# Kernel tuning notes

Measured on AMD Instinct MI355X. Metric: run time of the kernel, lower is better.

## Reference

```python
import jax, jax.numpy as jnp
import numpy as np
from jax import lax

B = 8192      # image batch
S = 32        # seq_length
I = 16        # ltc_input_size (sensory neurons)
U = 19        # ltc_hidden_size (units)
M = 2         # num_classes (motor neurons)
UNFOLDS = 6   # ncps LTCCell default ode_unfolds
EPS = 1e-8


def setup_inputs() -> dict:
    key = jax.random.key(0)
    ks = jax.random.split(key, 24)
    u = lambda k, sh, lo, hi: jax.random.uniform(k, sh, jnp.float32, lo, hi)
    x = jax.random.normal(ks[0], (B, 1, 28, 44), jnp.float32)
    conv1_w = jax.random.normal(ks[1], (6, 1, 5, 5), jnp.float32) * 0.2
    conv1_b = u(ks[2], (6,), -0.1, 0.1)
    conv2_w = jax.random.normal(ks[3], (16, 6, 5, 5), jnp.float32) * 0.08
    conv2_b = u(ks[4], (16,), -0.1, 0.1)
    # wiring adjacency (AutoNCP approximated by random sparse +/-1 polarity)
    sparsity_mask = (jax.random.uniform(ks[5], (U, U)) < 0.5).astype(jnp.float32)
    sensory_sparsity_mask = (jax.random.uniform(ks[6], (I, U)) < 0.5).astype(jnp.float32)
    erev = sparsity_mask * jnp.where(jax.random.uniform(ks[7], (U, U)) < 0.8, 1.0, -1.0)
    sensory_erev = sensory_sparsity_mask * jnp.where(jax.random.uniform(ks[8], (I, U)) < 0.8, 1.0, -1.0)
    # LTCCell parameter init ranges from ncps
    gleak = u(ks[9], (U,), 0.001, 1.0)
    vleak = u(ks[10], (U,), -0.2, 0.2)
    cm = u(ks[11], (U,), 0.4, 0.6)
    sigma = u(ks[12], (U, U), 3.0, 8.0)
    mu = u(ks[13], (U, U), 0.3, 0.8)
    w = u(ks[14], (U, U), 0.001, 1.0)
    sensory_sigma = u(ks[15], (I, U), 3.0, 8.0)
    sensory_mu = u(ks[16], (I, U), 0.3, 0.8)
    sensory_w = u(ks[17], (I, U), 0.001, 1.0)
    input_w = jnp.ones((I,), jnp.float32)
    input_b = jnp.zeros((I,), jnp.float32)
    output_w = jnp.ones((M,), jnp.float32)
    output_b = jnp.zeros((M,), jnp.float32)
    return dict(x=x, conv1_w=conv1_w, conv1_b=conv1_b, conv2_w=conv2_w, conv2_b=conv2_b,
                gleak=gleak, vleak=vleak, cm=cm, sigma=sigma, mu=mu, w=w, erev=erev,
                sensory_sigma=sensory_sigma, sensory_mu=sensory_mu, sensory_w=sensory_w,
                sensory_erev=sensory_erev, input_w=input_w, input_b=input_b,
                output_w=output_w, output_b=output_b,
                sparsity_mask=sparsity_mask, sensory_sparsity_mask=sensory_sparsity_mask)


def _maxpool2(h):
    return lax.reduce_window(h, -jnp.inf, lax.max, (1, 1, 2, 2), (1, 1, 2, 2), 'VALID')


def reference(x, conv1_w, conv1_b, conv2_w, conv2_b, gleak, vleak, cm, sigma, mu, w,
              erev, sensory_sigma, sensory_mu, sensory_w, sensory_erev, input_w, input_b,
              output_w, output_b, sparsity_mask, sensory_sparsity_mask):
    dn = ('NCHW', 'OIHW', 'NCHW')
    h = lax.conv_general_dilated(x, conv1_w, (1, 1), 'VALID', dimension_numbers=dn)
    h = _maxpool2(jax.nn.relu(h + conv1_b[None, :, None, None]))
    h = lax.conv_general_dilated(h, conv2_w, (1, 1), 'VALID', dimension_numbers=dn)
    h = _maxpool2(jax.nn.relu(h + conv2_b[None, :, None, None]))
    feat = h.reshape(h.shape[0], -1).reshape(-1, S, I)   # (B, 32, 16)
    seq = jnp.swapaxes(feat, 0, 1)                       # (S, B, I)
    cm_t = cm * UNFOLDS                                  # cm / (elapsed_time/unfolds), dt=1

    def step(v, inp):
        inp = inp * input_w + input_b                    # sensory affine mapping
        # sensory synapse activations (B, I, U), fixed over the ODE unfolds
        s_act = sensory_w * jax.nn.sigmoid(sensory_sigma * (inp[:, :, None] - sensory_mu))
        s_act = s_act * sensory_sparsity_mask
        w_num_s = jnp.sum(s_act * sensory_erev, axis=1)
        w_den_s = jnp.sum(s_act, axis=1)

        def unfold(vv, _):
            wa = w * jax.nn.sigmoid(sigma * (vv[:, :, None] - mu)) * sparsity_mask  # (B,U,U)
            num = cm_t * vv + gleak * vleak + jnp.sum(wa * erev, axis=1) + w_num_s
            den = cm_t + gleak + jnp.sum(wa, axis=1) + w_den_s
            return num / (den + EPS), None

        v, _ = lax.scan(unfold, v, None, length=UNFOLDS)
        return v, None

    v0 = jnp.zeros((feat.shape[0], U), x.dtype)
    vT, _ = lax.scan(step, v0, seq)
    # motor mapping: first M neurons, affine output map; equals out[:, -1, :]
    return vT[:, :M] * output_w + output_b
```

## Files before the change

kernel.cpp:

```cpp
#include <hip/hip_runtime.h>

#define BTOT 8192
#define SEQ 32
#define IPB 6
#define TPB 128
#define L2E 1.4426950408889634f
#define FSTRIDE 520
#define VSTRIDE 20

__global__ void prep_w2t(const float* __restrict__ w2, float* __restrict__ wt) {
    int idx = blockIdx.x * blockDim.x + threadIdx.x;
    if (idx < 2400) {
        int k = idx >> 4, c2 = idx & 15;
        wt[idx] = w2[c2 * 150 + k];
    }
}

__global__ __launch_bounds__(TPB, 3) void ltc_fused(
    const float* __restrict__ xin,
    const float* __restrict__ w1, const float* __restrict__ b1,
    const float* __restrict__ b2,
    const float* __restrict__ gleak, const float* __restrict__ vleak, const float* __restrict__ cm,
    const float* __restrict__ sigma, const float* __restrict__ mu, const float* __restrict__ ww,
    const float* __restrict__ erev,
    const float* __restrict__ ssigma, const float* __restrict__ smu, const float* __restrict__ sw,
    const float* __restrict__ serev,
    const float* __restrict__ inw, const float* __restrict__ inb,
    const float* __restrict__ outw, const float* __restrict__ outb,
    const float* __restrict__ mask, const float* __restrict__ smask,
    const float* __restrict__ wt,
    float* __restrict__ dout)
{
    __shared__ __align__(16) float uni[2736];
    __shared__ __align__(16) float featL[IPB * FSTRIDE];
    __shared__ __align__(16) float vbuf[IPB * VSTRIDE];
    __shared__ int ncol[19], mcol[19], cnts[2];

    float* img = uni;
    float* c1p = uni + 1232;
    float4* cR = (float4*)uni;
    float4* cS = ((float4*)uni) + 20 * 19;

    const int tid = threadIdx.x;
    const int b0 = blockIdx.x * IPB;

    for (int k = 0; k < IPB; ++k) {
        const int bG = b0 + k;
        const bool valid = bG < BTOT;
        if (valid) {
            for (int idx = tid; idx < 1232; idx += TPB) img[idx] = xin[bG * 1232 + idx];
        }
        __syncthreads();
        if (valid) {
            for (int idx = tid; idx < 240; idx += TPB) {
                int y = idx / 20, xx = idx - (idx / 20) * 20;
                const float* ib = img + (2 * y) * 44 + 2 * xx;
                float win[6][6];
                #pragma unroll
                for (int r = 0; r < 6; ++r) {
                    float2 a = *(const float2*)(ib + r * 44);
                    float2 b = *(const float2*)(ib + r * 44 + 2);
                    float2 c = *(const float2*)(ib + r * 44 + 4);
                    win[r][0] = a.x; win[r][1] = a.y; win[r][2] = b.x;
                    win[r][3] = b.y; win[r][4] = c.x; win[r][5] = c.y;
                }
                for (int ch = 0; ch < 6; ++ch) {
                    const float* wp = w1 + ch * 25;
                    float a00 = 0.f, a01 = 0.f, a10 = 0.f, a11 = 0.f;
                    #pragma unroll
                    for (int ky = 0; ky < 5; ++ky)
                        #pragma unroll
                        for (int kx = 0; kx < 5; ++kx) {
                            float wv = wp[ky * 5 + kx];
                            a00 = fmaf(wv, win[ky][kx], a00);
                            a01 = fmaf(wv, win[ky][kx + 1], a01);
                            a10 = fmaf(wv, win[ky + 1][kx], a10);
                            a11 = fmaf(wv, win[ky + 1][kx + 1], a11);
                        }
                    float m = fmaxf(fmaxf(a00, a01), fmaxf(a10, a11)) + b1[ch];
                    c1p[ch * 240 + idx] = fmaxf(m, 0.f);
                }
            }
        }
        __syncthreads();
        if (valid) {
            const int oy = tid >> 4, ox = tid & 15;
            float acc[16];
            #pragma unroll
            for (int c2 = 0; c2 < 16; ++c2) acc[c2] = 0.f;
            for (int ch = 0; ch < 6; ++ch) {
                const float* rowb = c1p + ch * 240 + oy * 20 + ox;
                const float* wch = wt + (ch * 25 << 4);
                #pragma unroll
                for (int ky = 0; ky < 5; ++ky) {
                    #pragma unroll
                    for (int kx = 0; kx < 5; ++kx) {
                        float xv = rowb[ky * 20 + kx];
                        const float4* wk = (const float4*)(wch + ((ky * 5 + kx) << 4));
                        float4 wa = wk[0], wb = wk[1], wc = wk[2], wd = wk[3];
                        acc[0]  = fmaf(wa.x, xv, acc[0]);  acc[1]  = fmaf(wa.y, xv, acc[1]);
                        acc[2]  = fmaf(wa.z, xv, acc[2]);  acc[3]  = fmaf(wa.w, xv, acc[3]);
                        acc[4]  = fmaf(wb.x, xv, acc[4]);  acc[5]  = fmaf(wb.y, xv, acc[5]);
                        acc[6]  = fmaf(wb.z, xv, acc[6]);  acc[7]  = fmaf(wb.w, xv, acc[7]);
                        acc[8]  = fmaf(wc.x, xv, acc[8]);  acc[9]  = fmaf(wc.y, xv, acc[9]);
                        acc[10] = fmaf(wc.z, xv, acc[10]); acc[11] = fmaf(wc.w, xv, acc[11]);
                        acc[12] = fmaf(wd.x, xv, acc[12]); acc[13] = fmaf(wd.y, xv, acc[13]);
                        acc[14] = fmaf(wd.z, xv, acc[14]); acc[15] = fmaf(wd.w, xv, acc[15]);
                    }
                }
            }
            const bool wl = ((tid & 1) == 0) && ((tid & 16) == 0);
            const int obase = k * FSTRIDE + (oy >> 1) * 8 + (ox >> 1);
            #pragma unroll
            for (int c2 = 0; c2 < 16; ++c2) {
                float a = acc[c2];
                a = fmaxf(a, __shfl_xor(a, 1));
                a = fmaxf(a, __shfl_xor(a, 16));
                if (wl) featL[obase + c2 * 32] = fmaxf(a + b2[c2], 0.f);
            }
        }
        __syncthreads();
    }

    for (int idx = tid; idx < 2736; idx += TPB) uni[idx] = 0.f;
    if (tid < IPB * VSTRIDE) vbuf[tid] = 0.f;
    __syncthreads();
    if (tid < 19) {
        const int j = tid;
        int c = 0;
        for (int i = 0; i < 19; ++i) {
            int idx = i * 19 + j;
            if (mask[idx] != 0.f) {
                float s = sigma[idx];
                cR[c * 19 + j] = make_float4(-L2E * s, L2E * s * mu[idx],
                                             ww[idx] * erev[idx], __int_as_float(i * 4));
                ++c;
            }
        }
        ncol[j] = c;
        c = 0;
        for (int i = 0; i < 16; ++i) {
            int idx = i * 19 + j;
            if (smask[idx] != 0.f) {
                float s = ssigma[idx];
                cS[c * 19 + j] = make_float4(-L2E * s * inw[i],
                                             -L2E * s * (inb[i] - smu[idx]),
                                             sw[idx] * serev[idx], __int_as_float(i * 4));
                ++c;
            }
        }
        mcol[j] = c;
    }
    __syncthreads();
    if (tid == 0) {
        int MR = 0, MS = 0;
        for (int j2 = 0; j2 < 19; ++j2) {
            MR = max(MR, ncol[j2]);
            MS = max(MS, mcol[j2]);
        }
        cnts[0] = (MR + 1) & ~1;
        cnts[1] = (MS + 1) & ~1;
    }
    __syncthreads();
    const int MR = __builtin_amdgcn_readfirstlane(cnts[0]);
    const int MS = __builtin_amdgcn_readfirstlane(cnts[1]);

    const int wv_ = tid >> 6, l = tid & 63;
    const int g = l / 19;
    const int j = l - g * 19;
    const int kimg = wv_ * 3 + g;
    const bool act = (g < 3) && (b0 + kimg < BTOT);
    const int kc = (kimg < IPB) ? kimg : (IPB - 1);

    const float gl = gleak[j];
    const float gv = gl * vleak[j];
    const float cmt = cm[j] * 6.f;

    float v = 0.f;
    const char* frowb = (const char*)(featL + kc * FSTRIDE);
    const char* vrowb = (const char*)(vbuf + kc * VSTRIDE);

    #pragma unroll 1
    for (int st = 0; st < SEQ; ++st) {
        const char* fb = frowb + (st << 6);
        float wns = 0.f, wds = 0.f;
        #pragma unroll 1
        for (int c = 0; c < MS; c += 2) {
            float4 pa = cS[c * 19 + j];
            float4 pb = cS[(c + 1) * 19 + j];
            float fa = *(const float*)(fb + __float_as_int(pa.w));
            float fbv = *(const float*)(fb + __float_as_int(pb.w));
            float ta = fmaf(pa.x, fa, pa.y);
            float tb = fmaf(pb.x, fbv, pb.y);
            float qa = 1.f + __builtin_amdgcn_exp2f(ta);
            float qb = 1.f + __builtin_amdgcn_exp2f(tb);
            float rr = __builtin_amdgcn_rcpf(qa * qb);
            float cn = fmaf(pa.z, qb, pb.z * qa);
            float cd = fmaf(fabsf(pa.z), qb, fabsf(pb.z) * qa);
            wns = fmaf(cn, rr, wns);
            wds = fmaf(cd, rr, wds);
        }
        const float nb = gv + wns;
        const float db = cmt + gl + wds;
        #pragma unroll 1
        for (int u = 0; u < 6; ++u) {
            float num = fmaf(cmt, v, nb);
            float den = db;
            #pragma unroll 1
            for (int c = 0; c < MR; c += 2) {
                float4 pa = cR[c * 19 + j];
                float4 pb = cR[(c + 1) * 19 + j];
                float va = *(const float*)(vrowb + __float_as_int(pa.w));
                float vb = *(const float*)(vrowb + __float_as_int(pb.w));
                float ta = fmaf(pa.x, va, pa.y);
                float tb = fmaf(pb.x, vb, pb.y);
                float qa = 1.f + __builtin_amdgcn_exp2f(ta);
                float qb = 1.f + __builtin_amdgcn_exp2f(tb);
                float rr = __builtin_amdgcn_rcpf(qa * qb);
                float cn = fmaf(pa.z, qb, pb.z * qa);
                float cd = fmaf(fabsf(pa.z), qb, fabsf(pb.z) * qa);
                num = fmaf(cn, rr, num);
                den = fmaf(cd, rr, den);
            }
            v = num * __builtin_amdgcn_rcpf(den + 1e-8f);
            __builtin_amdgcn_wave_barrier();
            __asm__ volatile("" ::: "memory");
            if (act) vbuf[kimg * VSTRIDE + j] = v;
            __builtin_amdgcn_wave_barrier();
            __asm__ volatile("" ::: "memory");
        }
    }
    if (act && j < 2) dout[(b0 + kimg) * 2 + j] = fmaf(v, outw[j], outb[j]);
}

extern "C" void kernel_launch(void* const* d_in, const int* in_sizes, int n_in,
                              void* d_out, int out_size, void* d_ws, size_t ws_size,
                              hipStream_t stream) {
    const float* x      = (const float*)d_in[0];
    const float* w1     = (const float*)d_in[1];
    const float* b1     = (const float*)d_in[2];
    const float* w2     = (const float*)d_in[3];
    const float* b2     = (const float*)d_in[4];
    const float* gleak  = (const float*)d_in[5];
    const float* vleak  = (const float*)d_in[6];
    const float* cm     = (const float*)d_in[7];
    const float* sigma  = (const float*)d_in[8];
    const float* mu     = (const float*)d_in[9];
    const float* ww     = (const float*)d_in[10];
    const float* erev   = (const float*)d_in[11];
    const float* ssig   = (const float*)d_in[12];
    const float* smu    = (const float*)d_in[13];
    const float* sw     = (const float*)d_in[14];
    const float* serev  = (const float*)d_in[15];
    const float* inw    = (const float*)d_in[16];
    const float* inb    = (const float*)d_in[17];
    const float* outw   = (const float*)d_in[18];
    const float* outb   = (const float*)d_in[19];
    const float* mask   = (const float*)d_in[20];
    const float* smask  = (const float*)d_in[21];
    float* wt = (float*)d_ws;

    hipLaunchKernelGGL(prep_w2t, dim3(10), dim3(256), 0, stream, w2, wt);

    dim3 grid((BTOT + IPB - 1) / IPB), block(TPB);
    hipLaunchKernelGGL(ltc_fused, grid, block, 0, stream,
                       x, w1, b1, b2, gleak, vleak, cm, sigma, mu, ww, erev,
                       ssig, smu, sw, serev, inw, inb, outw, outb, mask, smask,
                       (const float*)wt, (float*)d_out);
}
```

Measured before the change: 359.6 us.

## Cache recurrent synapse params in registers and exchange state via shuffles

The first 16 recurrent synapse entries per neuron are preloaded into registers as split A/B/weight/index arrays, and that inner ODE loop is fully unrolled. The per-unfold neuron state is read from other lanes with __shfl instead of being written to and read back from a shared vbuf. This removes the LDS round trip and its wave barriers. Parameters are stored as two float2 arrays, and the paired-sigmoid single-reciprocal trick is replaced by one reciprocal per synapse. This raises VGPR pressure and the number of transcendental ops in exchange for fewer LDS accesses and less loop overhead.

```diff
diff --git a/kernel.cpp b/kernel.cpp
--- a/kernel.cpp
+++ b/kernel.cpp
@@ -6,7 +6,7 @@
 #define TPB 128
 #define L2E 1.4426950408889634f
 #define FSTRIDE 520
-#define VSTRIDE 20
+#define RSL 16
 
 __global__ void prep_w2t(const float* __restrict__ w2, float* __restrict__ wt) {
     int idx = blockIdx.x * blockDim.x + threadIdx.x;
@@ -33,13 +33,14 @@
 {
     __shared__ __align__(16) float uni[2736];
     __shared__ __align__(16) float featL[IPB * FSTRIDE];
-    __shared__ __align__(16) float vbuf[IPB * VSTRIDE];
     __shared__ int ncol[19], mcol[19], cnts[2];
 
     float* img = uni;
     float* c1p = uni + 1232;
-    float4* cR = (float4*)uni;
-    float4* cS = ((float4*)uni) + 20 * 19;
+    float2* rAB = (float2*)uni;
+    float2* rZI = (float2*)(uni + 760);
+    float2* sAB = (float2*)(uni + 1520);
+    float2* sZI = (float2*)(uni + 2128);
 
     const int tid = threadIdx.x;
     const int b0 = blockIdx.x * IPB;
@@ -123,43 +124,42 @@
     }
 
     for (int idx = tid; idx < 2736; idx += TPB) uni[idx] = 0.f;
-    if (tid < IPB * VSTRIDE) vbuf[tid] = 0.f;
     __syncthreads();
     if (tid < 19) {
-        const int j = tid;
+        const int jj = tid;
         int c = 0;
         for (int i = 0; i < 19; ++i) {
-            int idx = i * 19 + j;
+            int idx = i * 19 + jj;
             if (mask[idx] != 0.f) {
                 float s = sigma[idx];
-                cR[c * 19 + j] = make_float4(-L2E * s, L2E * s * mu[idx],
-                                             ww[idx] * erev[idx], __int_as_float(i * 4));
+                rAB[c * 19 + jj] = make_float2(-L2E * s, L2E * s * mu[idx]);
+                rZI[c * 19 + jj] = make_float2(ww[idx] * erev[idx], __int_as_float(i));
                 ++c;
             }
         }
-        ncol[j] = c;
+        ncol[jj] = c;
         c = 0;
         for (int i = 0; i < 16; ++i) {
-            int idx = i * 19 + j;
+            int idx = i * 19 + jj;
             if (smask[idx] != 0.f) {
                 float s = ssigma[idx];
-                cS[c * 19 + j] = make_float4(-L2E * s * inw[i],
-                                             -L2E * s * (inb[i] - smu[idx]),
-                                             sw[idx] * serev[idx], __int_as_float(i * 4));
+                sAB[c * 19 + jj] = make_float2(-L2E * s * inw[i],
+                                               -L2E * s * (inb[i] - smu[idx]));
+                sZI[c * 19 + jj] = make_float2(sw[idx] * serev[idx], __int_as_float(i));
                 ++c;
             }
         }
-        mcol[j] = c;
+        mcol[jj] = c;
     }
     __syncthreads();
     if (tid == 0) {
-        int MR = 0, MS = 0;
+        int MRv = 0, MSv = 0;
         for (int j2 = 0; j2 < 19; ++j2) {
-            MR = max(MR, ncol[j2]);
-            MS = max(MS, mcol[j2]);
-        }
-        cnts[0] = (MR + 1) & ~1;
-        cnts[1] = (MS + 1) & ~1;
+            MRv = max(MRv, ncol[j2]);
+            MSv = max(MSv, mcol[j2]);
+        }
+        cnts[0] = MRv;
+        cnts[1] = MSv;
     }
     __syncthreads();
     const int MR = __builtin_amdgcn_readfirstlane(cnts[0]);
@@ -168,37 +168,46 @@
     const int wv_ = tid >> 6, l = tid & 63;
     const int g = l / 19;
     const int j = l - g * 19;
+    const int gbase = g * 19;
     const int kimg = wv_ * 3 + g;
     const bool act = (g < 3) && (b0 + kimg < BTOT);
     const int kc = (kimg < IPB) ? kimg : (IPB - 1);
 
+    float UA[RSL], UB[RSL], UZ[RSL];
+    int LI[RSL];
+    #pragma unroll
+    for (int c = 0; c < RSL; ++c) {
+        float2 ab = rAB[c * 19 + j];
+        float2 zi = rZI[c * 19 + j];
+        UA[c] = ab.x;
+        UB[c] = ab.y;
+        UZ[c] = zi.x;
+        LI[c] = gbase + __float_as_int(zi.y);
+    }
+    #pragma unroll
+    for (int c = 0; c < RSL; ++c)
+        asm volatile("" : "+v"(UA[c]), "+v"(UB[c]), "+v"(UZ[c]), "+v"(LI[c]));
+
     const float gl = gleak[j];
     const float gv = gl * vleak[j];
     const float cmt = cm[j] * 6.f;
 
     float v = 0.f;
-    const char* frowb = (const char*)(featL + kc * FSTRIDE);
-    const char* vrowb = (const char*)(vbuf + kc * VSTRIDE);
+    const float* frow = featL + kc * FSTRIDE;
 
     #pragma unroll 1
     for (int st = 0; st < SEQ; ++st) {
-        const char* fb = frowb + (st << 6);
+        const float* fb = frow + st * 16;
         float wns = 0.f, wds = 0.f;
         #pragma unroll 1
-        for (int c = 0; c < MS; c += 2) {
-            float4 pa = cS[c * 19 + j];
-            float4 pb = cS[(c + 1) * 19 + j];
-            float fa = *(const float*)(fb + __float_as_int(pa.w));
-            float fbv = *(const float*)(fb + __float_as_int(pb.w));
-            float ta = fmaf(pa.x, fa, pa.y);
-            float tb = fmaf(pb.x, fbv, pb.y);
-            float qa = 1.f + __builtin_amdgcn_exp2f(ta);
-            float qb = 1.f + __builtin_amdgcn_exp2f(tb);
-            float rr = __builtin_amdgcn_rcpf(qa * qb);
-            float cn = fmaf(pa.z, qb, pb.z * qa);
-            float cd = fmaf(fabsf(pa.z), qb, fabsf(pb.z) * qa);
-            wns = fmaf(cn, rr, wns);
-            wds = fmaf(cd, rr, wds);
+        for (int c = 0; c < MS; ++c) {
+            float2 ab = sAB[c * 19 + j];
+            float2 zi = sZI[c * 19 + j];
+            float f = fb[__float_as_int(zi.y)];
+            float t = fmaf(ab.x, f, ab.y);
+            float r = __builtin_amdgcn_rcpf(1.f + __builtin_amdgcn_exp2f(t));
+            wns = fmaf(zi.x, r, wns);
+            wds = fmaf(fabsf(zi.x), r, wds);
         }
         const float nb = gv + wns;
         const float db = cmt + gl + wds;
@@ -206,28 +215,25 @@
         for (int u = 0; u < 6; ++u) {
             float num = fmaf(cmt, v, nb);
             float den = db;
+            #pragma unroll
+            for (int c = 0; c < RSL; ++c) {
+                float vv = __shfl(v, LI[c]);
+                float t = fmaf(UA[c], vv, UB[c]);
+                float r = __builtin_amdgcn_rcpf(1.f + __builtin_amdgcn_exp2f(t));
+                num = fmaf(UZ[c], r, num);
+                den = fmaf(fabsf(UZ[c]), r, den);
+            }
             #pragma unroll 1
-            for (int c = 0; c < MR; c += 2) {
-                float4 pa = cR[c * 19 + j];
-                float4 pb = cR[(c + 1) * 19 + j];
-                float va = *(const float*)(vrowb + __float_as_int(pa.w));
-                float vb = *(const float*)(vrowb + __float_as_int(pb.w));
-                float ta = fmaf(pa.x, va, pa.y);
-                float tb = fmaf(pb.x, vb, pb.y);
-                float qa = 1.f + __builtin_amdgcn_exp2f(ta);
-                float qb = 1.f + __builtin_amdgcn_exp2f(tb);
-                float rr = __builtin_amdgcn_rcpf(qa * qb);
-                float cn = fmaf(pa.z, qb, pb.z * qa);
-                float cd = fmaf(fabsf(pa.z), qb, fabsf(pb.z) * qa);
-                num = fmaf(cn, rr, num);
-                den = fmaf(cd, rr, den);
+            for (int c = RSL; c < MR; ++c) {
+                float2 ab = rAB[c * 19 + j];
+                float2 zi = rZI[c * 19 + j];
+                float vv = __shfl(v, gbase + __float_as_int(zi.y));
+                float t = fmaf(ab.x, vv, ab.y);
+                float r = __builtin_amdgcn_rcpf(1.f + __builtin_amdgcn_exp2f(t));
+                num = fmaf(zi.x, r, num);
+                den = fmaf(fabsf(zi.x), r, den);
             }
             v = num * __builtin_amdgcn_rcpf(den + 1e-8f);
-            __builtin_amdgcn_wave_barrier();
-            __asm__ volatile("" ::: "memory");
-            if (act) vbuf[kimg * VSTRIDE + j] = v;
-            __builtin_amdgcn_wave_barrier();
-            __asm__ volatile("" ::: "memory");
         }
     }
     if (act && j < 2) dout[(b0 + kimg) * 2 + j] = fmaf(v, outw[j], outb[j]);
```

Measured after the change: 308.2 us. -14.3%, faster.
